# Kernel optimization log

Measured on AMD Instinct MI355X. Metric: run time of the kernel, lower is better.

The kernel has to match this reference:

```python
import jax, jax.numpy as jnp
import numpy as np

EPS = 1e-6

def _pixel_idx(loc_orig, H, W):
    # loc in [-1,1] -> nearest pixel, row-major flat index (matches 0.5*(loc+1)*[W,H]-0.5, round, clamp)
    xy = 0.5 * (loc_orig + 1.0) * jnp.array([W, H], dtype=loc_orig.dtype) - 0.5
    xy = jnp.round(xy).astype(jnp.int32)
    px = jnp.clip(xy[..., 0], 0, W - 1)
    py = jnp.clip(xy[..., 1], 0, H - 1)
    return py * W + px  # [B, N0]


def setup_inputs() -> dict:
    key = jax.random.key(0)
    ks = jax.random.split(key, 8)
    B, N, C = 4, 4096, 768
    H, W = 128, 128
    N0 = H * W
    x = jax.random.normal(ks[0], (B, N, C), dtype=jnp.float32)
    loc_orig = jax.random.uniform(ks[1], (B, N0, 2), minval=-1.0, maxval=1.0, dtype=jnp.float32)
    idx_agg = jax.random.randint(ks[2], (B, N0), 0, N, dtype=jnp.int32)
    agg_weight = jax.random.uniform(ks[3], (B, N0), dtype=jnp.float32)
    w_dw = jax.random.normal(ks[4], (C, 1, 3, 3), dtype=jnp.float32) * 0.1
    b_dw = jax.random.normal(ks[5], (C,), dtype=jnp.float32) * 0.1
    w_skip = jax.random.normal(ks[6], (C,), dtype=jnp.float32) * 0.1
    return {"x": x, "loc_orig": loc_orig, "idx_agg": idx_agg, "agg_weight": agg_weight,
            "H": H, "W": W, "w_dw": w_dw, "b_dw": b_dw, "w_skip": w_skip}


def reference(x, loc_orig, idx_agg, agg_weight, H, W, w_dw, b_dw, w_skip):
    B, N, C = x.shape
    N0 = loc_orig.shape[1]
    idx_hw = _pixel_idx(loc_orig, H, W)                      # [B, N0]
    boff = jnp.arange(B, dtype=jnp.int32)[:, None]
    seg_hw = (idx_hw + boff * (H * W)).reshape(-1)           # [B*N0] pixel segments
    seg_tok = (idx_agg.astype(jnp.int32) + boff * N).reshape(-1)  # [B*N0] token segments

    # token2map_agg_mat: scatter each orig position's token feature into its pixel, average by count
    feats = jnp.take_along_axis(x, idx_agg[..., None].astype(jnp.int32), axis=1).reshape(B * N0, C)
    sums = jax.ops.segment_sum(feats, seg_hw, num_segments=B * H * W)
    cnts = jax.ops.segment_sum(jnp.ones((B * N0,), x.dtype), seg_hw, num_segments=B * H * W)
    x_map = sums / (cnts + EPS)[:, None]
    x_map = x_map.reshape(B, H, W, C).transpose(0, 3, 1, 2)  # [B, C, H, W]

    # depthwise 3x3 conv (groups = C), padding 1, stride 1, with bias
    x_map = jax.lax.conv_general_dilated(
        x_map, w_dw, window_strides=(1, 1), padding=((1, 1), (1, 1)),
        dimension_numbers=("NCHW", "OIHW", "NCHW"), feature_group_count=C)
    x_map = x_map + b_dw[None, :, None, None]

    # map2token_agg_fast_nearest: weighted average of pixel feats per token
    pix = x_map.transpose(0, 2, 3, 1).reshape(B * H * W, C)[seg_hw]   # [B*N0, C]
    w = agg_weight.reshape(B * N0).astype(x.dtype)
    tok_sum = jax.ops.segment_sum(pix * w[:, None], seg_tok, num_segments=B * N)
    tok_w = jax.ops.segment_sum(w, seg_tok, num_segments=B * N)
    tok = (tok_sum / (tok_w + EPS)[:, None]).reshape(B, N, C)

    # grouped Conv1d(k=1, groups=C, bias=False) skip path == per-channel scale
    return tok + x * w_skip[None, None, :]
```

## Files before the change

### kernel.cpp

```cpp
#include <hip/hip_runtime.h>
#include <hip/hip_bf16.h>

#define BB 4
#define NN 4096
#define CC 768
#define HH 128
#define WW 128
#define N0 (HH * WW)
#define HW (HH * WW)
#define EPS 1e-6f
#define NSAMP (BB * N0)
#define NPIX  (BB * HW)
#define NTOK  (BB * NN)

#define TP 8
#define CSUB 128
#define TROWU 132
#define NTILE (HH / TP)
#define CONV_BLOCKS (BB * (CC / CSUB) * NTILE * NTILE)

#define XPB 4
#define TPB 4

__device__ inline float bf2f(ushort u) {
    unsigned v = ((unsigned)u) << 16;
    return __uint_as_float(v);
}
__device__ inline ushort f2bf(float f) {
    __hip_bfloat16 h = __float2bfloat16(f);
    return *reinterpret_cast<ushort*>(&h);
}
__device__ inline float4 us4_to_f4(ushort4 u) {
    float4 r;
    r.x = bf2f(u.x); r.y = bf2f(u.y); r.z = bf2f(u.z); r.w = bf2f(u.w);
    return r;
}

__global__ void k_idx(const float* __restrict__ loc,
                      const int* __restrict__ idx_agg,
                      int* __restrict__ idx_hw,
                      int* __restrict__ count_pix,
                      int* __restrict__ count_tok) {
    int i = blockIdx.x * blockDim.x + threadIdx.x;
    if (i >= NSAMP) return;
    float lx = loc[2 * i + 0];
    float ly = loc[2 * i + 1];
    float fx = 0.5f * (lx + 1.0f) * (float)WW - 0.5f;
    float fy = 0.5f * (ly + 1.0f) * (float)HH - 0.5f;
    int px = (int)rintf(fx);
    int py = (int)rintf(fy);
    px = min(max(px, 0), WW - 1);
    py = min(max(py, 0), HH - 1);
    int pix = py * WW + px;
    idx_hw[i] = pix;
    int b = i >> 14;
    atomicAdd(&count_pix[(b << 14) + pix], 1);
    atomicAdd(&count_tok[(b << 12) + idx_agg[i]], 1);
}

__global__ __launch_bounds__(1024) void k_scan(const int* __restrict__ cnt_pix,
                                               int* __restrict__ off_pix,
                                               const int* __restrict__ cnt_tok,
                                               int* __restrict__ off_tok) {
    __shared__ int wpart[16];
    __shared__ int run_sh;
    int bid = blockIdx.x;
    const int* cnt;
    int* off;
    int n, base, vbase;
    if (bid < 4) {
        cnt = cnt_pix; off = off_pix; n = HW;
        base = bid << 14; vbase = bid << 14;
    } else {
        cnt = cnt_tok; off = off_tok; n = NN;
        base = (bid - 4) << 12; vbase = (bid - 4) << 14;
    }
    int t = threadIdx.x;
    int lane = t & 63;
    int wid = t >> 6;
    if (t == 0) run_sh = 0;
    __syncthreads();
    for (int it = 0; it < n; it += 1024) {
        int idx = it + t;
        int v = (idx < n) ? cnt[base + idx] : 0;
        int s = v;
#pragma unroll
        for (int d = 1; d < 64; d <<= 1) {
            int u = __shfl_up(s, d, 64);
            if (lane >= d) s += u;
        }
        if (lane == 63) wpart[wid] = s;
        __syncthreads();
        if (wid == 0) {
            int p = (lane < 16) ? wpart[lane] : 0;
#pragma unroll
            for (int d = 1; d < 16; d <<= 1) {
                int u = __shfl_up(p, d, 64);
                if (lane >= d) p += u;
            }
            if (lane < 16) wpart[lane] = p;
        }
        __syncthreads();
        int wbase = (wid == 0) ? 0 : wpart[wid - 1];
        int run = run_sh;
        if (idx < n) off[base + idx] = vbase + run + wbase + s - v;
        __syncthreads();
        if (t == 0) run_sh = run + wpart[15];
        __syncthreads();
    }
}

__global__ void k_fill(const int* __restrict__ idx_hw,
                       const int* __restrict__ idx_agg,
                       const int* __restrict__ off_pix, int* __restrict__ fill_pix,
                       int* __restrict__ list_pix,
                       const int* __restrict__ off_tok, int* __restrict__ fill_tok,
                       int* __restrict__ list_tok) {
    int i = blockIdx.x * blockDim.x + threadIdx.x;
    if (i >= NSAMP) return;
    int b = i >> 14;
    int sp = (b << 14) + idx_hw[i];
    int p = atomicAdd(&fill_pix[sp], 1);
    list_pix[off_pix[sp] + p] = i;
    int st = (b << 12) + idx_agg[i];
    int q = atomicAdd(&fill_tok[st], 1);
    list_tok[off_tok[st] + q] = i;
}

__global__ __launch_bounds__(192) void k_xmap(const float* __restrict__ x,
                                              const int* __restrict__ idx_agg,
                                              const int* __restrict__ count_pix,
                                              const int* __restrict__ off_pix,
                                              const int* __restrict__ list_pix,
                                              ushort* __restrict__ xm) {
    int bi0 = blockIdx.x * XPB;
    int b = bi0 >> 14;
    int c4 = threadIdx.x;
    const float* xb = x + (size_t)(b * NN) * CC;

    int kk[XPB], st[XPB];
#pragma unroll
    for (int p = 0; p < XPB; ++p) {
        kk[p] = count_pix[bi0 + p];
        st[p] = off_pix[bi0 + p];
    }
    float4 acc[XPB];
#pragma unroll
    for (int p = 0; p < XPB; ++p) acc[p] = make_float4(0.f, 0.f, 0.f, 0.f);

    int kmax = max(max(kk[0], kk[1]), max(kk[2], kk[3]));
    for (int j = 0; j < kmax; ++j) {
#pragma unroll
        for (int p = 0; p < XPB; ++p) {
            if (j < kk[p]) {
                int i = list_pix[st[p] + j];
                int tok = idx_agg[i];
                float4 v = ((const float4*)(xb + (size_t)tok * CC))[c4];
                acc[p].x += v.x; acc[p].y += v.y;
                acc[p].z += v.z; acc[p].w += v.w;
            }
        }
    }
#pragma unroll
    for (int p = 0; p < XPB; ++p) {
        float inv = 1.0f / ((float)kk[p] + EPS);
        ushort4 o;
        o.x = f2bf(acc[p].x * inv); o.y = f2bf(acc[p].y * inv);
        o.z = f2bf(acc[p].z * inv); o.w = f2bf(acc[p].w * inv);
        ((ushort4*)(xm + (size_t)(bi0 + p) * CC))[c4] = o;
    }
}

__global__ __launch_bounds__(256, 4) void k_conv(const ushort* __restrict__ xm,
                                                 const float* __restrict__ w_dw,
                                                 const float* __restrict__ b_dw,
                                                 ushort* __restrict__ ym) {
    __shared__ ushort tile[(TP + 2) * (TP + 2) * TROWU];

    int f = blockIdx.x;
    f = (f & 7) * (CONV_BLOCKS / 8) + (f >> 3);
    int tx = f & 15;
    int ty = (f >> 4) & 15;
    int cblk = (f >> 8) % 6;
    int b = f / 1536;
    int tid = threadIdx.x;

    int c0g = cblk * CSUB;
    const ushort* src = xm + (size_t)(b << 14) * CC + c0g;

    for (int idx = tid; idx < (TP + 2) * (TP + 2) * (CSUB / 4); idx += 256) {
        int lc = idx & 31;
        int cell = idx >> 5;
        int r = cell / (TP + 2);
        int c = cell % (TP + 2);
        int gy = ty * TP + r - 1;
        int gx = tx * TP + c - 1;
        ushort4 v = {0, 0, 0, 0};
        if (gy >= 0 && gy < HH && gx >= 0 && gx < WW) {
            v = ((const ushort4*)(src + (size_t)(gy * WW + gx) * CC))[lc];
        }
        ((ushort4*)(tile + (size_t)cell * TROWU))[lc] = v;
    }
    __syncthreads();

    int c4 = tid & 31;
    int px = tid >> 5;

    float wreg[36];
    {
        const float4* wp = (const float4*)(w_dw + (size_t)(c0g + c4 * 4) * 9);
#pragma unroll
        for (int j = 0; j < 9; ++j) ((float4*)wreg)[j] = wp[j];
    }
    float4 bias = ((const float4*)(b_dw + c0g))[c4];

    float4 a[3][3];
#pragma unroll
    for (int i = 0; i < 2; ++i)
#pragma unroll
        for (int j = 0; j < 3; ++j)
            a[i][j] = us4_to_f4(((const ushort4*)(tile + (size_t)(i * (TP + 2) + px + j) * TROWU))[c4]);

    ushort* dst_base = ym + (size_t)((b << 14) + (ty * TP) * WW + tx * TP + px) * CC
                       + c0g;

#pragma unroll
    for (int oy = 0; oy < TP; ++oy) {
#pragma unroll
        for (int j = 0; j < 3; ++j)
            a[2][j] = us4_to_f4(((const ushort4*)(tile + (size_t)((oy + 2) * (TP + 2) + px + j) * TROWU))[c4]);

        float4 acc = bias;
#pragma unroll
        for (int i = 0; i < 3; ++i) {
#pragma unroll
            for (int j = 0; j < 3; ++j) {
                int t = i * 3 + j;
                acc.x += a[i][j].x * wreg[0 * 9 + t];
                acc.y += a[i][j].y * wreg[1 * 9 + t];
                acc.z += a[i][j].z * wreg[2 * 9 + t];
                acc.w += a[i][j].w * wreg[3 * 9 + t];
            }
        }
        ushort4 o;
        o.x = f2bf(acc.x); o.y = f2bf(acc.y); o.z = f2bf(acc.z); o.w = f2bf(acc.w);
        ((ushort4*)(dst_base + (size_t)oy * WW * CC))[c4] = o;

#pragma unroll
        for (int j = 0; j < 3; ++j) {
            a[0][j] = a[1][j];
            a[1][j] = a[2][j];
        }
    }
}

__global__ __launch_bounds__(192) void k_token(const ushort* __restrict__ ym,
                                               const float* __restrict__ x,
                                               const float* __restrict__ agg_w,
                                               const int* __restrict__ idx_hw,
                                               const int* __restrict__ count_tok,
                                               const int* __restrict__ off_tok,
                                               const int* __restrict__ list_tok,
                                               const float* __restrict__ w_skip,
                                               float* __restrict__ out) {
    int bi0 = blockIdx.x * TPB;
    int b = bi0 >> 12;
    int c4 = threadIdx.x;
    const ushort* yb = ym + (size_t)(b << 14) * CC;

    int kk[TPB], st[TPB];
#pragma unroll
    for (int p = 0; p < TPB; ++p) {
        kk[p] = count_tok[bi0 + p];
        st[p] = off_tok[bi0 + p];
    }
    float4 acc[TPB];
    float tw[TPB];
#pragma unroll
    for (int p = 0; p < TPB; ++p) {
        acc[p] = make_float4(0.f, 0.f, 0.f, 0.f);
        tw[p] = 0.f;
    }

    int kmax = max(max(kk[0], kk[1]), max(kk[2], kk[3]));
    for (int j = 0; j < kmax; ++j) {
#pragma unroll
        for (int p = 0; p < TPB; ++p) {
            if (j < kk[p]) {
                int i = list_tok[st[p] + j];
                float w = agg_w[i];
                int pix = idx_hw[i];
                float4 v = us4_to_f4(((const ushort4*)(yb + (size_t)pix * CC))[c4]);
                acc[p].x += w * v.x; acc[p].y += w * v.y;
                acc[p].z += w * v.z; acc[p].w += w * v.w;
                tw[p] += w;
            }
        }
    }

    float4 ws = ((const float4*)w_skip)[c4];
#pragma unroll
    for (int p = 0; p < TPB; ++p) {
        float inv = 1.0f / (tw[p] + EPS);
        float4 xv = ((const float4*)(x + (size_t)(bi0 + p) * CC))[c4];
        float4 o;
        o.x = acc[p].x * inv + xv.x * ws.x;
        o.y = acc[p].y * inv + xv.y * ws.y;
        o.z = acc[p].z * inv + xv.z * ws.z;
        o.w = acc[p].w * inv + xv.w * ws.w;
        ((float4*)(out + (size_t)(bi0 + p) * CC))[c4] = o;
    }
}

extern "C" void kernel_launch(void* const* d_in, const int* in_sizes, int n_in,
                              void* d_out, int out_size, void* d_ws, size_t ws_size,
                              hipStream_t stream) {
    const float* x       = (const float*)d_in[0];
    const float* loc     = (const float*)d_in[1];
    const int*   idx_agg = (const int*)d_in[2];
    const float* agg_w   = (const float*)d_in[3];
    const float* w_dw    = (const float*)d_in[6];
    const float* b_dw    = (const float*)d_in[7];
    const float* w_skip  = (const float*)d_in[8];
    float* out = (float*)d_out;
    char* ws = (char*)d_ws;

    size_t off = 0;
    int* count_pix = (int*)(ws + off); off += (size_t)NPIX * 4;
    int* fill_pix  = (int*)(ws + off); off += (size_t)NPIX * 4;
    int* count_tok = (int*)(ws + off); off += (size_t)NTOK * 4;
    int* fill_tok  = (int*)(ws + off); off += (size_t)NTOK * 4;
    size_t zero_bytes = off;
    int* idx_hw   = (int*)(ws + off); off += (size_t)NSAMP * 4;
    int* off_pix  = (int*)(ws + off); off += (size_t)NPIX * 4;
    int* list_pix = (int*)(ws + off); off += (size_t)NSAMP * 4;
    int* off_tok  = (int*)(ws + off); off += (size_t)NTOK * 4;
    int* list_tok = (int*)(ws + off); off += (size_t)NSAMP * 4;
    ushort* xm = (ushort*)(ws + off); off += (size_t)NPIX * CC * 2;
    ushort* ym = (ushort*)(ws + off); off += (size_t)NPIX * CC * 2;

    hipMemsetAsync(ws, 0, zero_bytes, stream);

    hipLaunchKernelGGL(k_idx, dim3(NSAMP / 256), dim3(256), 0, stream,
                       loc, idx_agg, idx_hw, count_pix, count_tok);
    hipLaunchKernelGGL(k_scan, dim3(8), dim3(1024), 0, stream,
                       count_pix, off_pix, count_tok, off_tok);
    hipLaunchKernelGGL(k_fill, dim3(NSAMP / 256), dim3(256), 0, stream,
                       idx_hw, idx_agg, off_pix, fill_pix, list_pix,
                       off_tok, fill_tok, list_tok);
    hipLaunchKernelGGL(k_xmap, dim3(NPIX / XPB), dim3(192), 0, stream,
                       x, idx_agg, count_pix, off_pix, list_pix, xm);
    hipLaunchKernelGGL(k_conv, dim3(CONV_BLOCKS), dim3(256), 0, stream,
                       xm, w_dw, b_dw, ym);
    hipLaunchKernelGGL(k_token, dim3(NTOK / TPB), dim3(192), 0, stream,
                       ym, x, agg_w, idx_hw, count_tok, off_tok, list_tok,
                       w_skip, out);
}
```

Before: 172.7 us.

## Fuse pixel-map gather into depthwise conv tile load, dropping intermediate map buffer

Removes the separate scatter-average kernel. The conv kernel now builds its haloed shared-memory tile directly by gathering token features per pixel and averaging, with channel groups widened to 256. This avoids writing and re-reading the bf16 intermediate pixel map in global memory. In exchange, halo pixels are gathered redundantly by neighbouring tiles, and the per-thread serial list walks may expose gather latency.

```diff
diff --git a/kernel.cpp b/kernel.cpp
--- a/kernel.cpp
+++ b/kernel.cpp
@@ -14,12 +14,11 @@
 #define NTOK  (BB * NN)
 
 #define TP 8
-#define CSUB 128
-#define TROWU 132
+#define CSUBF 256
+#define TROWF 260
 #define NTILE (HH / TP)
-#define CONV_BLOCKS (BB * (CC / CSUB) * NTILE * NTILE)
-
-#define XPB 4
+#define FCONV_BLOCKS (BB * (CC / CSUBF) * NTILE * NTILE)
+
 #define TPB 4
 
 __device__ inline float bf2f(ushort u) {
@@ -127,130 +126,110 @@
     list_tok[off_tok[st] + q] = i;
 }
 
-__global__ __launch_bounds__(192) void k_xmap(const float* __restrict__ x,
-                                              const int* __restrict__ idx_agg,
-                                              const int* __restrict__ count_pix,
-                                              const int* __restrict__ off_pix,
-                                              const int* __restrict__ list_pix,
-                                              ushort* __restrict__ xm) {
-    int bi0 = blockIdx.x * XPB;
-    int b = bi0 >> 14;
-    int c4 = threadIdx.x;
-    const float* xb = x + (size_t)(b * NN) * CC;
-
-    int kk[XPB], st[XPB];
-#pragma unroll
-    for (int p = 0; p < XPB; ++p) {
-        kk[p] = count_pix[bi0 + p];
-        st[p] = off_pix[bi0 + p];
-    }
-    float4 acc[XPB];
-#pragma unroll
-    for (int p = 0; p < XPB; ++p) acc[p] = make_float4(0.f, 0.f, 0.f, 0.f);
-
-    int kmax = max(max(kk[0], kk[1]), max(kk[2], kk[3]));
-    for (int j = 0; j < kmax; ++j) {
-#pragma unroll
-        for (int p = 0; p < XPB; ++p) {
-            if (j < kk[p]) {
-                int i = list_pix[st[p] + j];
-                int tok = idx_agg[i];
-                float4 v = ((const float4*)(xb + (size_t)tok * CC))[c4];
-                acc[p].x += v.x; acc[p].y += v.y;
-                acc[p].z += v.z; acc[p].w += v.w;
-            }
-        }
-    }
-#pragma unroll
-    for (int p = 0; p < XPB; ++p) {
-        float inv = 1.0f / ((float)kk[p] + EPS);
-        ushort4 o;
-        o.x = f2bf(acc[p].x * inv); o.y = f2bf(acc[p].y * inv);
-        o.z = f2bf(acc[p].z * inv); o.w = f2bf(acc[p].w * inv);
-        ((ushort4*)(xm + (size_t)(bi0 + p) * CC))[c4] = o;
-    }
-}
-
-__global__ __launch_bounds__(256, 4) void k_conv(const ushort* __restrict__ xm,
-                                                 const float* __restrict__ w_dw,
-                                                 const float* __restrict__ b_dw,
-                                                 ushort* __restrict__ ym) {
-    __shared__ ushort tile[(TP + 2) * (TP + 2) * TROWU];
+__global__ __launch_bounds__(256, 3) void k_fconv(const float* __restrict__ x,
+                                                  const int* __restrict__ idx_agg,
+                                                  const int* __restrict__ count_pix,
+                                                  const int* __restrict__ off_pix,
+                                                  const int* __restrict__ list_pix,
+                                                  const float* __restrict__ w_dw,
+                                                  const float* __restrict__ b_dw,
+                                                  ushort* __restrict__ ym) {
+    __shared__ ushort tile[(TP + 2) * (TP + 2) * TROWF];
 
     int f = blockIdx.x;
-    f = (f & 7) * (CONV_BLOCKS / 8) + (f >> 3);
+    f = (f & 7) * (FCONV_BLOCKS / 8) + (f >> 3);
     int tx = f & 15;
     int ty = (f >> 4) & 15;
-    int cblk = (f >> 8) % 6;
-    int b = f / 1536;
+    int cg = (f >> 8) % 3;
+    int b = f / 768;
     int tid = threadIdx.x;
 
-    int c0g = cblk * CSUB;
-    const ushort* src = xm + (size_t)(b << 14) * CC + c0g;
-
-    for (int idx = tid; idx < (TP + 2) * (TP + 2) * (CSUB / 4); idx += 256) {
-        int lc = idx & 31;
-        int cell = idx >> 5;
+    int c0g = cg * CSUBF;
+    const float* xb = x + (size_t)(b * NN) * CC + c0g;
+
+    for (int task = tid; task < (TP + 2) * (TP + 2) * (CSUBF / 4); task += 256) {
+        int slot = task & 63;
+        int cell = task >> 6;
         int r = cell / (TP + 2);
         int c = cell % (TP + 2);
         int gy = ty * TP + r - 1;
         int gx = tx * TP + c - 1;
-        ushort4 v = {0, 0, 0, 0};
+        float4 acc = {0.f, 0.f, 0.f, 0.f};
+        float inv = 0.f;
         if (gy >= 0 && gy < HH && gx >= 0 && gx < WW) {
-            v = ((const ushort4*)(src + (size_t)(gy * WW + gx) * CC))[lc];
-        }
-        ((ushort4*)(tile + (size_t)cell * TROWU))[lc] = v;
+            int bi = (b << 14) + gy * WW + gx;
+            int k = count_pix[bi];
+            int st = off_pix[bi];
+            for (int j = 0; j < k; ++j) {
+                int i = list_pix[st + j];
+                int tok = idx_agg[i];
+                float4 v = ((const float4*)(xb + (size_t)tok * CC))[slot];
+                acc.x += v.x; acc.y += v.y; acc.z += v.z; acc.w += v.w;
+            }
+            inv = 1.0f / ((float)k + EPS);
+        }
+        ushort4 o;
+        o.x = f2bf(acc.x * inv); o.y = f2bf(acc.y * inv);
+        o.z = f2bf(acc.z * inv); o.w = f2bf(acc.w * inv);
+        ((ushort4*)(tile + (size_t)cell * TROWF))[slot] = o;
     }
     __syncthreads();
 
     int c4 = tid & 31;
     int px = tid >> 5;
 
-    float wreg[36];
-    {
-        const float4* wp = (const float4*)(w_dw + (size_t)(c0g + c4 * 4) * 9);
-#pragma unroll
-        for (int j = 0; j < 9; ++j) ((float4*)wreg)[j] = wp[j];
-    }
-    float4 bias = ((const float4*)(b_dw + c0g))[c4];
-
-    float4 a[3][3];
-#pragma unroll
-    for (int i = 0; i < 2; ++i)
-#pragma unroll
-        for (int j = 0; j < 3; ++j)
-            a[i][j] = us4_to_f4(((const ushort4*)(tile + (size_t)(i * (TP + 2) + px + j) * TROWU))[c4]);
-
-    ushort* dst_base = ym + (size_t)((b << 14) + (ty * TP) * WW + tx * TP + px) * CC
-                       + c0g;
-
-#pragma unroll
-    for (int oy = 0; oy < TP; ++oy) {
-#pragma unroll
-        for (int j = 0; j < 3; ++j)
-            a[2][j] = us4_to_f4(((const ushort4*)(tile + (size_t)((oy + 2) * (TP + 2) + px + j) * TROWU))[c4]);
-
-        float4 acc = bias;
-#pragma unroll
-        for (int i = 0; i < 3; ++i) {
+#pragma unroll
+    for (int h = 0; h < 2; ++h) {
+        int cofs = h * 128 + c4 * 4;
+        int uslot = h * 32 + c4;
+
+        float wreg[36];
+        {
+            const float4* wp = (const float4*)(w_dw + (size_t)(c0g + cofs) * 9);
+#pragma unroll
+            for (int j = 0; j < 9; ++j) ((float4*)wreg)[j] = wp[j];
+        }
+        float4 bias = ((const float4*)(b_dw + c0g + cofs))[0];
+
+        float4 a[3][3];
+#pragma unroll
+        for (int i = 0; i < 2; ++i)
+#pragma unroll
+            for (int j = 0; j < 3; ++j)
+                a[i][j] = us4_to_f4(((const ushort4*)(tile + (size_t)(i * (TP + 2) + px + j) * TROWF))[uslot]);
+
+        ushort* dst_base = ym + (size_t)((b << 14) + (ty * TP) * WW + tx * TP + px) * CC
+                           + c0g + cofs;
+
+#pragma unroll
+        for (int oy = 0; oy < TP; ++oy) {
+#pragma unroll
+            for (int j = 0; j < 3; ++j)
+                a[2][j] = us4_to_f4(((const ushort4*)(tile + (size_t)((oy + 2) * (TP + 2) + px + j) * TROWF))[uslot]);
+
+            float4 acc = bias;
+#pragma unroll
+            for (int i = 0; i < 3; ++i) {
+#pragma unroll
+                for (int j = 0; j < 3; ++j) {
+                    int t = i * 3 + j;
+                    acc.x += a[i][j].x * wreg[0 * 9 + t];
+                    acc.y += a[i][j].y * wreg[1 * 9 + t];
+                    acc.z += a[i][j].z * wreg[2 * 9 + t];
+                    acc.w += a[i][j].w * wreg[3 * 9 + t];
+                }
+            }
+            ushort4 o;
+            o.x = f2bf(acc.x); o.y = f2bf(acc.y); o.z = f2bf(acc.z); o.w = f2bf(acc.w);
+            ((ushort4*)(dst_base + (size_t)oy * WW * CC))[0] = o;
+
 #pragma unroll
             for (int j = 0; j < 3; ++j) {
-                int t = i * 3 + j;
-                acc.x += a[i][j].x * wreg[0 * 9 + t];
-                acc.y += a[i][j].y * wreg[1 * 9 + t];
-                acc.z += a[i][j].z * wreg[2 * 9 + t];
-                acc.w += a[i][j].w * wreg[3 * 9 + t];
-            }
-        }
-        ushort4 o;
-        o.x = f2bf(acc.x); o.y = f2bf(acc.y); o.z = f2bf(acc.z); o.w = f2bf(acc.w);
-        ((ushort4*)(dst_base + (size_t)oy * WW * CC))[c4] = o;
-
-#pragma unroll
-        for (int j = 0; j < 3; ++j) {
-            a[0][j] = a[1][j];
-            a[1][j] = a[2][j];
-        }
+                a[0][j] = a[1][j];
+                a[1][j] = a[2][j];
+            }
+        }
+        if (h == 0) {  }
     }
 }
 
@@ -336,7 +315,6 @@
     int* list_pix = (int*)(ws + off); off += (size_t)NSAMP * 4;
     int* off_tok  = (int*)(ws + off); off += (size_t)NTOK * 4;
     int* list_tok = (int*)(ws + off); off += (size_t)NSAMP * 4;
-    ushort* xm = (ushort*)(ws + off); off += (size_t)NPIX * CC * 2;
     ushort* ym = (ushort*)(ws + off); off += (size_t)NPIX * CC * 2;
 
     hipMemsetAsync(ws, 0, zero_bytes, stream);
@@ -348,10 +326,8 @@
     hipLaunchKernelGGL(k_fill, dim3(NSAMP / 256), dim3(256), 0, stream,
                        idx_hw, idx_agg, off_pix, fill_pix, list_pix,
                        off_tok, fill_tok, list_tok);
-    hipLaunchKernelGGL(k_xmap, dim3(NPIX / XPB), dim3(192), 0, stream,
-                       x, idx_agg, count_pix, off_pix, list_pix, xm);
-    hipLaunchKernelGGL(k_conv, dim3(CONV_BLOCKS), dim3(256), 0, stream,
-                       xm, w_dw, b_dw, ym);
+    hipLaunchKernelGGL(k_fconv, dim3(FCONV_BLOCKS), dim3(256), 0, stream,
+                       x, idx_agg, count_pix, off_pix, list_pix, w_dw, b_dw, ym);
     hipLaunchKernelGGL(k_token, dim3(NTOK / TPB), dim3(192), 0, stream,
                        ym, x, agg_w, idx_hw, count_tok, off_tok, list_tok,
                        w_skip, out);
```

Result: slower. 205.2 us (+18.8%).
